# Optimization experiments

Measured on AMD Instinct MI355X. Metric: run time of the kernel, lower is better.

The kernel has to match this reference:

```python
import jax, jax.numpy as jnp
import numpy as np

N = 50000            # nodes
E = 800000           # random edges (self loops added in reference, per PyG default)
D_IN, D1, D2, D_OUT = 256, 128, 64, 40
SLOPE = 0.2          # GATv2Conv default negative_slope


def _glorot(key, shape):
    fan_in, fan_out = shape[0], shape[-1]
    s = jnp.sqrt(6.0 / (fan_in + fan_out))
    return jax.random.uniform(key, shape, jnp.float32, -s, s)


def setup_inputs() -> dict:
    key = jax.random.key(0)
    ks = jax.random.split(key, 16)
    inp = {
        "x": jax.random.normal(ks[0], (N, D_IN), jnp.float32),
        "edge_index": jax.random.randint(ks[1], (2, E), 0, N),
    }
    dims = [(D_IN, D1), (D1, D2), (D2, D_OUT)]
    k = 2
    for i, (di, do) in enumerate(dims, 1):
        inp[f"W{i}l"] = _glorot(ks[k], (di, do)); k += 1
        inp[f"W{i}r"] = _glorot(ks[k], (di, do)); k += 1
        inp[f"b{i}l"] = jnp.zeros((do,), jnp.float32)
        inp[f"b{i}r"] = jnp.zeros((do,), jnp.float32)
        inp[f"a{i}"]  = _glorot(ks[k], (do,));    k += 1
        inp[f"c{i}"]  = jnp.zeros((do,), jnp.float32)
    return inp


def _gatv2(x, src, dst, Wl, bl, Wr, br, att, bias):
    # GATv2Conv, heads=1: lin_l on source nodes, lin_r on target nodes
    xl = x @ Wl + bl                     # [N, do] source transform
    xr = x @ Wr + br                     # [N, do] target transform
    e = jax.nn.leaky_relu(xl[src] + xr[dst], SLOPE)   # [Etot, do]
    logits = e @ att                     # [Etot]
    # segment softmax over incoming edges of each dst node
    m = jax.ops.segment_max(logits, dst, num_segments=N)
    ex = jnp.exp(logits - m[dst])
    denom = jax.ops.segment_sum(ex, dst, num_segments=N)
    alpha = ex / denom[dst]              # [Etot]
    out = jax.ops.segment_sum(alpha[:, None] * xl[src], dst, num_segments=N)
    return out + bias


def reference(x, edge_index,
              W1l, W1r, b1l, b1r, a1, c1,
              W2l, W2r, b2l, b2r, a2, c2,
              W3l, W3r, b3l, b3r, a3, c3):
    loop = jnp.arange(N, dtype=edge_index.dtype)
    src = jnp.concatenate([edge_index[0], loop])   # add_self_loops=True
    dst = jnp.concatenate([edge_index[1], loop])
    h = jax.nn.relu(_gatv2(x, src, dst, W1l, b1l, W1r, b1r, a1, c1))
    h = jax.nn.relu(_gatv2(h, src, dst, W2l, b2l, W2r, b2r, a2, c2))
    h = _gatv2(h, src, dst, W3l, b3l, W3r, b3r, a3, c3)
    return jax.nn.log_softmax(h, axis=1)
```

## Files before the change

kernel.cpp:

```cpp
#include <hip/hip_runtime.h>
#include <math.h>

#define NN 50000
#define NE 800000
#define SLOPE 0.2f
#define NEGX (-1e30f)
#define CH 8192

typedef _Float16 h8 __attribute__((ext_vector_type(8)));
typedef _Float16 h4 __attribute__((ext_vector_type(4)));
typedef _Float16 h2 __attribute__((ext_vector_type(2)));
typedef float f8 __attribute__((ext_vector_type(8)));
typedef float v4f __attribute__((ext_vector_type(4)));

__device__ __forceinline__ h8 hzero(){ h8 z = {0,0,0,0,0,0,0,0}; return z; }

__device__ __forceinline__ void pack_one(const float* __restrict__ W,
                                         _Float16* __restrict__ Wp,
                                         int DO, int K, int NT, int t){
  int KC = K >> 5;
  if (t >= NT * KC * 64) return;
  int lane = t & 63;
  int rest = t >> 6;
  int c  = rest % KC;
  int nt = rest / KC;
  int col = nt * 16 + (lane & 15);
  int k0  = c * 32 + ((lane >> 4) << 3);
  _Float16 o[8];
#pragma unroll
  for (int j = 0; j < 8; j++){
    float v = (col < DO) ? W[(k0 + j) * DO + col] : 0.f;
    o[j] = (_Float16)v;
  }
  *(ulonglong2*)(Wp + (size_t)t * 8) = *(ulonglong2*)o;
}

__global__ __launch_bounds__(256) void k_pack_hist(
    const float* W1l, const float* W1r, const float* W2l,
    const float* W2r, const float* W3l, const float* W3r,
    _Float16* p1l, _Float16* p1r, _Float16* p2l,
    _Float16* p2r, _Float16* p3l, _Float16* p3r,
    const int* __restrict__ ei, int* __restrict__ gbp){
  __shared__ int h[256];
  int b = blockIdx.x, t = threadIdx.x;
  if (b < 44){
    if      (b < 16) pack_one(W1l, p1l, 128, 256, 8, (b     ) * 256 + t);
    else if (b < 32) pack_one(W1r, p1r, 128, 256, 8, (b - 16) * 256 + t);
    else if (b < 36) pack_one(W2l, p2l,  64, 128, 4, (b - 32) * 256 + t);
    else if (b < 40) pack_one(W2r, p2r,  64, 128, 4, (b - 36) * 256 + t);
    else if (b < 42) pack_one(W3l, p3l,  40,  64, 3, (b - 40) * 256 + t);
    else             pack_one(W3r, p3r,  40,  64, 3, (b - 42) * 256 + t);
  } else {
    int hb = b - 44;
    h[t] = 0;
    __syncthreads();
    int e0 = hb * 12500;
    for (int i = t; i < 12500; i += 256)
      atomicAdd(&h[ei[NE + e0 + i] >> 8], 1);
    __syncthreads();
    gbp[hb * 256 + t] = h[t];
  }
}

__global__ __launch_bounds__(256) void k_scan(const int* __restrict__ gbp,
                                              int* __restrict__ base,
                                              int* __restrict__ bcur,
                                              int* __restrict__ row_ptr){
  __shared__ int s[256];
  int t = threadIdx.x;
  int v = 0;
#pragma unroll 8
  for (int i = 0; i < 64; i++) v += gbp[i * 256 + t];
  s[t] = v; __syncthreads();
  for (int off = 1; off < 256; off <<= 1){
    int a = (t >= off) ? s[t - off] : 0;
    __syncthreads(); s[t] += a; __syncthreads();
  }
  int ex = s[t] - v;
  base[t] = ex;
  bcur[t] = ex;
  if (t == 255){ base[256] = s[255]; row_ptr[NN] = s[255]; }
}

__global__ __launch_bounds__(256) void k_bscatter(const int* __restrict__ ei,
                                                  int* __restrict__ bcur,
                                                  unsigned* __restrict__ pk_out){
  __shared__ unsigned pk[CH];
  __shared__ int h[256];
  int t = threadIdx.x;
  int e0 = blockIdx.x * CH;
  h[t] = 0;
  __syncthreads();
  int n = NE - e0; if (n > CH) n = CH;
  for (int i = t; i < n; i += 256){
    int e = e0 + i;
    int s = ei[e], d = ei[NE + e];
    pk[i] = (unsigned)s | ((unsigned)(d & 255) << 16) | ((unsigned)(d >> 8) << 24);
    atomicAdd(&h[d >> 8], 1);
  }
  __syncthreads();
  int c = h[t];
  if (c) h[t] = atomicAdd(&bcur[t], c);
  __syncthreads();
  for (int i = t; i < n; i += 256){
    unsigned u = pk[i];
    int pos = atomicAdd(&h[u >> 24], 1);
    pk_out[pos] = u;
  }
}

__global__ __launch_bounds__(256) void k_bcsr(const unsigned* __restrict__ pk,
                                              const int* __restrict__ base,
                                              int* __restrict__ row_ptr,
                                              int* __restrict__ csr_src){
  __shared__ int h[256], s[256];
  int t = threadIdx.x;
  int b = blockIdx.x;
  int lo = base[b], hi = base[b + 1];
  h[t] = 0;
  __syncthreads();
  for (int i = lo + t; i < hi; i += 256)
    atomicAdd(&h[(pk[i] >> 16) & 255], 1);
  __syncthreads();
  int v = h[t];
  s[t] = v; __syncthreads();
  for (int off = 1; off < 256; off <<= 1){
    int a = (t >= off) ? s[t - off] : 0;
    __syncthreads(); s[t] += a; __syncthreads();
  }
  int ex = lo + s[t] - v;
  int node = b * 256 + t;
  if (node < NN) row_ptr[node] = ex;
  h[t] = ex;
  __syncthreads();
  for (int i = lo + t; i < hi; i += 256){
    unsigned u = pk[i];
    int pos = atomicAdd(&h[(u >> 16) & 255], 1);
    csr_src[pos] = (int)(u & 0xFFFFu);
  }
}

template<typename TI, int K, int DO>
__global__ __launch_bounds__(256, 4) void gemm_direct(
    const TI* __restrict__ X,
    const _Float16* __restrict__ Wpl, const float* __restrict__ bl,
    const _Float16* __restrict__ Wpr, const float* __restrict__ br,
    _Float16* __restrict__ Yl, _Float16* __restrict__ Yr)
{
  constexpr int KC = K / 32;
  constexpr int NT = (DO + 15) / 16;
  int lane = threadIdx.x & 63;
  int wv   = threadIdx.x >> 6;
  int row0 = (blockIdx.x * 4 + wv) * 16;
  int arow = lane & 15;
  int koff = lane >> 4;
  int lrow = row0 + arow;
  int crow = (lrow < NN) ? lrow : 0;

  h8 afrag[KC];
  if constexpr (sizeof(TI) == 4){
    const float* Xr = (const float*)X + (size_t)crow * K + koff * 8;
#pragma unroll
    for (int c = 0; c < KC; c++){
      float4 v0 = *reinterpret_cast<const float4*>(Xr + c * 32);
      float4 v1 = *reinterpret_cast<const float4*>(Xr + c * 32 + 4);
      h8 a;
      a[0]=(_Float16)v0.x; a[1]=(_Float16)v0.y; a[2]=(_Float16)v0.z; a[3]=(_Float16)v0.w;
      a[4]=(_Float16)v1.x; a[5]=(_Float16)v1.y; a[6]=(_Float16)v1.z; a[7]=(_Float16)v1.w;
      afrag[c] = a;
    }
  } else {
    const _Float16* Xr = (const _Float16*)X + (size_t)crow * K + koff * 8;
#pragma unroll
    for (int c = 0; c < KC; c++)
      afrag[c] = *reinterpret_cast<const h8*>(Xr + c * 32);
  }

#pragma unroll
  for (int side = 0; side < 2; side++){
    const _Float16* Wp = side ? Wpr : Wpl;
    const float* bias = side ? br : bl;
    _Float16* Y = side ? Yr : Yl;
#pragma unroll
    for (int nt = 0; nt < NT; nt++){
      v4f acc = {0.f, 0.f, 0.f, 0.f};
#pragma unroll
      for (int c = 0; c < KC; c++){
        h8 b = *reinterpret_cast<const h8*>(Wp + (size_t)((nt * KC + c) * 64 + lane) * 8);
        acc = __builtin_amdgcn_mfma_f32_16x16x32_f16(afrag[c], b, acc, 0, 0, 0);
      }
      int col = nt * 16 + arow;
      if (col < DO){
        float bv = bias[col];
        int rbase = row0 + koff * 4;
#pragma unroll
        for (int r = 0; r < 4; r++){
          int orow = rbase + r;
          if (orow < NN) Y[(size_t)orow * DO + col] = (_Float16)(acc[r] + bv);
        }
      }
    }
  }
}

__device__ __forceinline__ float edge_logit(h8 x, h8 xrv, h8 attv){
  h8 t = x + xrv;
  h8 l = __builtin_elementwise_max(t, t * (_Float16)SLOPE);
  const h2* lp = (const h2*)&l;
  const h2* ap = (const h2*)&attv;
  h2 d = lp[0] * ap[0];
  d += lp[1] * ap[1];
  d += lp[2] * ap[2];
  d += lp[3] * ap[3];
  return (float)d[0] + (float)d[1];
}

template<int LPG>
__device__ __forceinline__ float gsum(float v){
#pragma unroll
  for (int off = 1; off < LPG; off <<= 1) v += __shfl_xor(v, off, 64);
  return v;
}
template<int LPG>
__device__ __forceinline__ void gsum2(float& a, float& b){
#pragma unroll
  for (int off = 1; off < LPG; off <<= 1){
    a += __shfl_xor(a, off, 64);
    b += __shfl_xor(b, off, 64);
  }
}
template<int LPG>
__device__ __forceinline__ float gmax(float v){
#pragma unroll
  for (int off = 1; off < LPG; off <<= 1) v = fmaxf(v, __shfl_xor(v, off, 64));
  return v;
}

template<int DO, int LPG, int ACT, typename OT>
__global__ __launch_bounds__(256) void gat_agg(
    const _Float16* __restrict__ xl, const _Float16* __restrict__ xr,
    const int* __restrict__ csr_src, const int* __restrict__ row_ptr,
    const float* __restrict__ att, const float* __restrict__ bias,
    OT* __restrict__ out)
{
  constexpr int G = 64 / LPG;
  int lane = threadIdx.x & 63;
  int wv = (blockIdx.x * 256 + threadIdx.x) >> 6;
  int g = lane / LPG;
  int p = lane % LPG;
  int node = wv * G + g;
  if (node >= NN) return;
  int cbase = p * 8;
  bool ok = (LPG * 8 <= DO) ? true : (cbase < DO);

  h8 attv = hzero(), xrv = hzero(), xlv = hzero();
  if (ok){
    float4 a0 = *reinterpret_cast<const float4*>(att + cbase);
    float4 a1 = *reinterpret_cast<const float4*>(att + cbase + 4);
    attv[0]=(_Float16)a0.x; attv[1]=(_Float16)a0.y; attv[2]=(_Float16)a0.z; attv[3]=(_Float16)a0.w;
    attv[4]=(_Float16)a1.x; attv[5]=(_Float16)a1.y; attv[6]=(_Float16)a1.z; attv[7]=(_Float16)a1.w;
    xrv = *reinterpret_cast<const h8*>(xr + node * DO + cbase);
    xlv = *reinterpret_cast<const h8*>(xl + node * DO + cbase);
  }

  float s = gsum<LPG>(edge_logit(xlv, xrv, attv));
  float wS = __expf(s);
  float denA = wS, denB = 0.f;
  float accA[8], accB[8];
  {
    f8 xf = __builtin_convertvector(xlv, f8);
#pragma unroll
    for (int j = 0; j < 8; j++){ accA[j] = wS * xf[j]; accB[j] = 0.f; }
  }

  int e0 = row_ptr[node], e1 = row_ptr[node + 1];
  int e = e0;
  for (; e + 1 < e1; e += 2){
    int sA = csr_src[e], sB = csr_src[e + 1];
    h8 xA = ok ? *reinterpret_cast<const h8*>(xl + sA * DO + cbase) : hzero();
    h8 xB = ok ? *reinterpret_cast<const h8*>(xl + sB * DO + cbase) : hzero();
    float pA = edge_logit(xA, xrv, attv);
    float pB = edge_logit(xB, xrv, attv);
    gsum2<LPG>(pA, pB);
    float wA = __expf(pA), wB = __expf(pB);
    denA += wA; denB += wB;
    f8 fA = __builtin_convertvector(xA, f8);
    f8 fB = __builtin_convertvector(xB, f8);
#pragma unroll
    for (int j = 0; j < 8; j++){
      accA[j] = fmaf(wA, fA[j], accA[j]);
      accB[j] = fmaf(wB, fB[j], accB[j]);
    }
  }
  if (e < e1){
    int sA = csr_src[e];
    h8 xA = ok ? *reinterpret_cast<const h8*>(xl + sA * DO + cbase) : hzero();
    float pA = gsum<LPG>(edge_logit(xA, xrv, attv));
    float w = __expf(pA);
    denA += w;
    f8 fA = __builtin_convertvector(xA, f8);
#pragma unroll
    for (int j = 0; j < 8; j++) accA[j] = fmaf(w, fA[j], accA[j]);
  }

  float inv = 1.0f / (denA + denB);
  if (ACT == 0){
    if (ok){
      f8 vv;
#pragma unroll
      for (int j = 0; j < 4; j++){
        float bj;
        bj = bias[cbase + j];     vv[j]   = fmaxf(fmaf(accA[j] + accB[j], inv, bj), 0.f);
        bj = bias[cbase + 4 + j]; vv[4+j] = fmaxf(fmaf(accA[4+j] + accB[4+j], inv, bj), 0.f);
      }
      h8 o = __builtin_convertvector(vv, h8);
      *reinterpret_cast<h8*>((_Float16*)out + node * DO + cbase) = o;
    }
  } else {
    float v[8]; float lmax = NEGX;
#pragma unroll
    for (int j = 0; j < 8; j++){
      v[j] = ok ? fmaf(accA[j] + accB[j], inv, bias[cbase + j]) : NEGX;
      lmax = fmaxf(lmax, v[j]);
    }
    lmax = gmax<LPG>(lmax);
    float lsum = 0.f;
#pragma unroll
    for (int j = 0; j < 8; j++) lsum += __expf(v[j] - lmax);
    lsum = gsum<LPG>(lsum);
    if (ok){
      float lg = lmax + __logf(lsum);
      float* op = (float*)out + node * DO + cbase;
      float4 o0, o1;
      o0.x = v[0] - lg; o0.y = v[1] - lg; o0.z = v[2] - lg; o0.w = v[3] - lg;
      o1.x = v[4] - lg; o1.y = v[5] - lg; o1.z = v[6] - lg; o1.w = v[7] - lg;
      *reinterpret_cast<float4*>(op) = o0;
      *reinterpret_cast<float4*>(op + 4) = o1;
    }
  }
}

extern "C" void kernel_launch(void* const* d_in, const int* in_sizes, int n_in,
                              void* d_out, int out_size, void* d_ws, size_t ws_size,
                              hipStream_t stream) {
  const float* x   = (const float*)d_in[0];
  const int*   ei  = (const int*)d_in[1];
  const float* W1l = (const float*)d_in[2];  const float* W1r = (const float*)d_in[3];
  const float* b1l = (const float*)d_in[4];  const float* b1r = (const float*)d_in[5];
  const float* a1  = (const float*)d_in[6];  const float* c1  = (const float*)d_in[7];
  const float* W2l = (const float*)d_in[8];  const float* W2r = (const float*)d_in[9];
  const float* b2l = (const float*)d_in[10]; const float* b2r = (const float*)d_in[11];
  const float* a2  = (const float*)d_in[12]; const float* c2  = (const float*)d_in[13];
  const float* W3l = (const float*)d_in[14]; const float* W3r = (const float*)d_in[15];
  const float* b3l = (const float*)d_in[16]; const float* b3r = (const float*)d_in[17];
  const float* a3  = (const float*)d_in[18]; const float* c3  = (const float*)d_in[19];
  float* outp = (float*)d_out;

  _Float16* xl = (_Float16*)d_ws;
  _Float16* xr = xl + 6400000;
  _Float16* h1 = xr + 6400000;
  _Float16* h2 = h1 + 6400000;
  _Float16* wp1l = h2 + 3200000;
  _Float16* wp1r = wp1l + 32768;
  _Float16* wp2l = wp1r + 32768;
  _Float16* wp2r = wp2l + 8192;
  _Float16* wp3l = wp2r + 8192;
  _Float16* wp3r = wp3l + 3072;
  unsigned* pk   = (unsigned*)(wp3r + 3072);
  int* csr_src   = (int*)(pk + NE);
  int* row_ptr   = csr_src + NE;
  int* gbp       = row_ptr + 50001;
  int* base      = gbp + 16384;
  int* bcur      = base + 257;

  const int GB = (NN + 63) / 64;
  const int SB = (NE + CH - 1) / CH;
  const int AB1 = (NN + 15) / 16;
  const int AB2 = (NN + 31) / 32;

  k_pack_hist<<<108, 256, 0, stream>>>(W1l, W1r, W2l, W2r, W3l, W3r,
                                       wp1l, wp1r, wp2l, wp2r, wp3l, wp3r,
                                       ei, gbp);
  k_scan<<<1, 256, 0, stream>>>(gbp, base, bcur, row_ptr);
  k_bscatter<<<SB, 256, 0, stream>>>(ei, bcur, pk);
  k_bcsr<<<196, 256, 0, stream>>>(pk, base, row_ptr, csr_src);

  gemm_direct<float,256,128><<<GB, 256, 0, stream>>>(x, wp1l, b1l, wp1r, b1r, xl, xr);
  gat_agg<128,16,0,_Float16><<<AB1, 256, 0, stream>>>(xl, xr, csr_src, row_ptr, a1, c1, h1);

  gemm_direct<_Float16,128,64><<<GB, 256, 0, stream>>>(h1, wp2l, b2l, wp2r, b2r, xl, xr);
  gat_agg<64,8,0,_Float16><<<AB2, 256, 0, stream>>>(xl, xr, csr_src, row_ptr, a2, c2, h2);

  gemm_direct<_Float16,64,40><<<GB, 256, 0, stream>>>(h2, wp3l, b3l, wp3r, b3r, xl, xr);
  gat_agg<40,8,1,float><<<AB2, 256, 0, stream>>>(xl, xr, csr_src, row_ptr, a3, c3, outp);
}
```

Baseline: 296.7 us.

## Fuse GAT aggregation with next layer's linear transforms via LDS and MFMA

Layers 1 and 2 now finish their aggregation by writing the activated hidden rows into shared memory, then run the next layer's left and right projections with MFMA inside the same block. This removes the round trip of writing h1 and h2 to global memory and reading them back in separate GEMM kernels, along with two kernel launches. Each layer gets its own xl/xr buffers. In exchange the fused blocks add a barrier and use only a few MFMA tiles per block. The row stores to Yl/Yr are scattered 2-byte writes rather than vectorized ones.

```diff
diff --git a/kernel.cpp b/kernel.cpp
--- a/kernel.cpp
+++ b/kernel.cpp
@@ -8,7 +8,6 @@
 #define CH 8192
 
 typedef _Float16 h8 __attribute__((ext_vector_type(8)));
-typedef _Float16 h4 __attribute__((ext_vector_type(4)));
 typedef _Float16 h2 __attribute__((ext_vector_type(2)));
 typedef float f8 __attribute__((ext_vector_type(8)));
 typedef float v4f __attribute__((ext_vector_type(4)));
@@ -236,12 +235,134 @@
   return v;
 }
 
-template<int DO, int LPG, int ACT, typename OT>
-__global__ __launch_bounds__(256) void gat_agg(
+template<int DO, int LPG, int DO2>
+__global__ __launch_bounds__(256) void agg_gemm(
     const _Float16* __restrict__ xl, const _Float16* __restrict__ xr,
     const int* __restrict__ csr_src, const int* __restrict__ row_ptr,
     const float* __restrict__ att, const float* __restrict__ bias,
-    OT* __restrict__ out)
+    const _Float16* __restrict__ Wpl2, const float* __restrict__ bl2,
+    const _Float16* __restrict__ Wpr2, const float* __restrict__ br2,
+    _Float16* __restrict__ Yl, _Float16* __restrict__ Yr)
+{
+  constexpr int G = 64 / LPG;
+  constexpr int NPB = 4 * G;
+  constexpr int LK = DO + 8;
+  constexpr int KC2 = DO / 32;
+  constexpr int NT2 = (DO2 + 15) / 16;
+  constexpr int MT = NPB / 16;
+  __shared__ _Float16 hs[NPB * LK];
+
+  int lane = threadIdx.x & 63;
+  int wid  = threadIdx.x >> 6;
+  int g = lane / LPG, p = lane % LPG;
+  int nodeLocal = wid * G + g;
+  int node = blockIdx.x * NPB + nodeLocal;
+  int cbase = p * 8;
+  bool nvalid = node < NN;
+  int nodeC = nvalid ? node : 0;
+
+  h8 attv, xrv, xlv;
+  {
+    float4 a0 = *reinterpret_cast<const float4*>(att + cbase);
+    float4 a1 = *reinterpret_cast<const float4*>(att + cbase + 4);
+    attv[0]=(_Float16)a0.x; attv[1]=(_Float16)a0.y; attv[2]=(_Float16)a0.z; attv[3]=(_Float16)a0.w;
+    attv[4]=(_Float16)a1.x; attv[5]=(_Float16)a1.y; attv[6]=(_Float16)a1.z; attv[7]=(_Float16)a1.w;
+    xrv = *reinterpret_cast<const h8*>(xr + nodeC * DO + cbase);
+    xlv = *reinterpret_cast<const h8*>(xl + nodeC * DO + cbase);
+  }
+  float s = gsum<LPG>(edge_logit(xlv, xrv, attv));
+  float wS = __expf(s);
+  float denA = wS, denB = 0.f;
+  float accA[8], accB[8];
+  {
+    f8 xf = __builtin_convertvector(xlv, f8);
+#pragma unroll
+    for (int j = 0; j < 8; j++){ accA[j] = wS * xf[j]; accB[j] = 0.f; }
+  }
+
+  int e0 = row_ptr[nodeC];
+  int e1 = nvalid ? row_ptr[nodeC + 1] : e0;
+  int e = e0;
+  for (; e + 1 < e1; e += 2){
+    int sA = csr_src[e], sB = csr_src[e + 1];
+    h8 xA = *reinterpret_cast<const h8*>(xl + sA * DO + cbase);
+    h8 xB = *reinterpret_cast<const h8*>(xl + sB * DO + cbase);
+    float pA = edge_logit(xA, xrv, attv);
+    float pB = edge_logit(xB, xrv, attv);
+    gsum2<LPG>(pA, pB);
+    float wA = __expf(pA), wB = __expf(pB);
+    denA += wA; denB += wB;
+    f8 fA = __builtin_convertvector(xA, f8);
+    f8 fB = __builtin_convertvector(xB, f8);
+#pragma unroll
+    for (int j = 0; j < 8; j++){
+      accA[j] = fmaf(wA, fA[j], accA[j]);
+      accB[j] = fmaf(wB, fB[j], accB[j]);
+    }
+  }
+  if (e < e1){
+    int sA = csr_src[e];
+    h8 xA = *reinterpret_cast<const h8*>(xl + sA * DO + cbase);
+    float pA = gsum<LPG>(edge_logit(xA, xrv, attv));
+    float w = __expf(pA);
+    denA += w;
+    f8 fA = __builtin_convertvector(xA, f8);
+#pragma unroll
+    for (int j = 0; j < 8; j++) accA[j] = fmaf(w, fA[j], accA[j]);
+  }
+
+  {
+    float inv = 1.0f / (denA + denB);
+    f8 vv;
+#pragma unroll
+    for (int j = 0; j < 8; j++)
+      vv[j] = fmaxf(fmaf(accA[j] + accB[j], inv, bias[cbase + j]), 0.f);
+    h8 ho = __builtin_convertvector(vv, h8);
+    *reinterpret_cast<h8*>(&hs[nodeLocal * LK + cbase]) = ho;
+  }
+  __syncthreads();
+
+  int arow = lane & 15;
+  int koff = lane >> 4;
+  int mt = (MT == 1) ? 0 : (wid >> 1);
+  h8 afrag[KC2];
+#pragma unroll
+  for (int c = 0; c < KC2; c++)
+    afrag[c] = *reinterpret_cast<const h8*>(&hs[(mt * 16 + arow) * LK + koff * 8 + c * 32]);
+
+  int row0 = blockIdx.x * NPB + mt * 16;
+  int side = wid & 1;
+  const _Float16* Wp = side ? Wpr2 : Wpl2;
+  const float* bias2 = side ? br2 : bl2;
+  _Float16* Y = side ? Yr : Yl;
+  int nt_begin = (MT == 1) ? (wid >> 1) * (NT2 / 2) : 0;
+  int nt_end   = (MT == 1) ? nt_begin + NT2 / 2 : NT2;
+  for (int nt = nt_begin; nt < nt_end; nt++){
+    v4f acc = {0.f, 0.f, 0.f, 0.f};
+#pragma unroll
+    for (int c = 0; c < KC2; c++){
+      h8 b = *reinterpret_cast<const h8*>(Wp + (size_t)((nt * KC2 + c) * 64 + lane) * 8);
+      acc = __builtin_amdgcn_mfma_f32_16x16x32_f16(afrag[c], b, acc, 0, 0, 0);
+    }
+    int col = nt * 16 + arow;
+    if (col < DO2){
+      float bv = bias2[col];
+      int rbase = row0 + koff * 4;
+#pragma unroll
+      for (int r = 0; r < 4; r++){
+        int orow = rbase + r;
+        if (orow < NN) Y[(size_t)orow * DO2 + col] = (_Float16)(acc[r] + bv);
+      }
+    }
+  }
+}
+
+template<int DO, int LPG>
+__global__ __launch_bounds__(256) void gat_agg_out(
+    const _Float16* __restrict__ xl, const _Float16* __restrict__ xr,
+    const int* __restrict__ csr_src, const int* __restrict__ row_ptr,
+    const float* __restrict__ att, const float* __restrict__ bias,
+    float* __restrict__ out)
 {
   constexpr int G = 64 / LPG;
   int lane = threadIdx.x & 63;
@@ -251,7 +372,7 @@
   int node = wv * G + g;
   if (node >= NN) return;
   int cbase = p * 8;
-  bool ok = (LPG * 8 <= DO) ? true : (cbase < DO);
+  bool ok = (cbase < DO);
 
   h8 attv = hzero(), xrv = hzero(), xlv = hzero();
   if (ok){
@@ -304,39 +425,25 @@
   }
 
   float inv = 1.0f / (denA + denB);
-  if (ACT == 0){
-    if (ok){
-      f8 vv;
-#pragma unroll
-      for (int j = 0; j < 4; j++){
-        float bj;
-        bj = bias[cbase + j];     vv[j]   = fmaxf(fmaf(accA[j] + accB[j], inv, bj), 0.f);
-        bj = bias[cbase + 4 + j]; vv[4+j] = fmaxf(fmaf(accA[4+j] + accB[4+j], inv, bj), 0.f);
-      }
-      h8 o = __builtin_convertvector(vv, h8);
-      *reinterpret_cast<h8*>((_Float16*)out + node * DO + cbase) = o;
-    }
-  } else {
-    float v[8]; float lmax = NEGX;
-#pragma unroll
-    for (int j = 0; j < 8; j++){
-      v[j] = ok ? fmaf(accA[j] + accB[j], inv, bias[cbase + j]) : NEGX;
-      lmax = fmaxf(lmax, v[j]);
-    }
-    lmax = gmax<LPG>(lmax);
-    float lsum = 0.f;
-#pragma unroll
-    for (int j = 0; j < 8; j++) lsum += __expf(v[j] - lmax);
-    lsum = gsum<LPG>(lsum);
-    if (ok){
-      float lg = lmax + __logf(lsum);
-      float* op = (float*)out + node * DO + cbase;
-      float4 o0, o1;
-      o0.x = v[0] - lg; o0.y = v[1] - lg; o0.z = v[2] - lg; o0.w = v[3] - lg;
-      o1.x = v[4] - lg; o1.y = v[5] - lg; o1.z = v[6] - lg; o1.w = v[7] - lg;
-      *reinterpret_cast<float4*>(op) = o0;
-      *reinterpret_cast<float4*>(op + 4) = o1;
-    }
+  float v[8]; float lmax = NEGX;
+#pragma unroll
+  for (int j = 0; j < 8; j++){
+    v[j] = ok ? fmaf(accA[j] + accB[j], inv, bias[cbase + j]) : NEGX;
+    lmax = fmaxf(lmax, v[j]);
+  }
+  lmax = gmax<LPG>(lmax);
+  float lsum = 0.f;
+#pragma unroll
+  for (int j = 0; j < 8; j++) lsum += __expf(v[j] - lmax);
+  lsum = gsum<LPG>(lsum);
+  if (ok){
+    float lg = lmax + __logf(lsum);
+    float* op = (float*)out + node * DO + cbase;
+    float4 o0, o1;
+    o0.x = v[0] - lg; o0.y = v[1] - lg; o0.z = v[2] - lg; o0.w = v[3] - lg;
+    o1.x = v[4] - lg; o1.y = v[5] - lg; o1.z = v[6] - lg; o1.w = v[7] - lg;
+    *reinterpret_cast<float4*>(op) = o0;
+    *reinterpret_cast<float4*>(op + 4) = o1;
   }
 }
 
@@ -356,11 +463,13 @@
   const float* a3  = (const float*)d_in[18]; const float* c3  = (const float*)d_in[19];
   float* outp = (float*)d_out;
 
-  _Float16* xl = (_Float16*)d_ws;
-  _Float16* xr = xl + 6400000;
-  _Float16* h1 = xr + 6400000;
-  _Float16* h2 = h1 + 6400000;
-  _Float16* wp1l = h2 + 3200000;
+  _Float16* xl1 = (_Float16*)d_ws;
+  _Float16* xr1 = xl1 + 6400000;
+  _Float16* xl2 = xr1 + 6400000;
+  _Float16* xr2 = xl2 + 3200000;
+  _Float16* xl3 = xr2 + 3200000;
+  _Float16* xr3 = xl3 + 2000000;
+  _Float16* wp1l = xr3 + 2000000;
   _Float16* wp1r = wp1l + 32768;
   _Float16* wp2l = wp1r + 32768;
   _Float16* wp2r = wp2l + 8192;
@@ -375,8 +484,9 @@
 
   const int GB = (NN + 63) / 64;
   const int SB = (NE + CH - 1) / CH;
-  const int AB1 = (NN + 15) / 16;
-  const int AB2 = (NN + 31) / 32;
+  const int FB1 = (NN + 15) / 16;
+  const int FB2 = (NN + 31) / 32;
+  const int AB3 = (NN + 31) / 32;
 
   k_pack_hist<<<108, 256, 0, stream>>>(W1l, W1r, W2l, W2r, W3l, W3r,
                                        wp1l, wp1r, wp2l, wp2r, wp3l, wp3r,
@@ -385,12 +495,13 @@
   k_bscatter<<<SB, 256, 0, stream>>>(ei, bcur, pk);
   k_bcsr<<<196, 256, 0, stream>>>(pk, base, row_ptr, csr_src);
 
-  gemm_direct<float,256,128><<<GB, 256, 0, stream>>>(x, wp1l, b1l, wp1r, b1r, xl, xr);
-  gat_agg<128,16,0,_Float16><<<AB1, 256, 0, stream>>>(xl, xr, csr_src, row_ptr, a1, c1, h1);
-
-  gemm_direct<_Float16,128,64><<<GB, 256, 0, stream>>>(h1, wp2l, b2l, wp2r, b2r, xl, xr);
-  gat_agg<64,8,0,_Float16><<<AB2, 256, 0, stream>>>(xl, xr, csr_src, row_ptr, a2, c2, h2);
-
-  gemm_direct<_Float16,64,40><<<GB, 256, 0, stream>>>(h2, wp3l, b3l, wp3r, b3r, xl, xr);
-  gat_agg<40,8,1,float><<<AB2, 256, 0, stream>>>(xl, xr, csr_src, row_ptr, a3, c3, outp);
-}
+  gemm_direct<float,256,128><<<GB, 256, 0, stream>>>(x, wp1l, b1l, wp1r, b1r, xl1, xr1);
+
+  agg_gemm<128,16,64><<<FB1, 256, 0, stream>>>(xl1, xr1, csr_src, row_ptr,
+                                               a1, c1, wp2l, b2l, wp2r, b2r, xl2, xr2);
+
+  agg_gemm<64,8,40><<<FB2, 256, 0, stream>>>(xl2, xr2, csr_src, row_ptr,
+                                             a2, c2, wp3l, b3l, wp3r, b3r, xl3, xr3);
+
+  gat_agg_out<40,8><<<AB3, 256, 0, stream>>>(xl3, xr3, csr_src, row_ptr, a3, c3, outp);
+}
```

Result: faster. 286.9 us (-3.3%).
